# Kernel tuning notes

Measured on AMD Instinct MI355X. Metric: run time of the kernel, lower is better.

Reference implementation:

```python
import jax, jax.numpy as jnp
import numpy as np

S = 520   # WAP_SIZE / sequence length
E = 6     # EMBEDDING_SIZE
H = 3     # num_heads
D = 2     # head_dim
EPS = 1e-5


def _layer_norm(x, g, b):
    m = jnp.mean(x, axis=-1, keepdims=True)
    v = jnp.mean((x - m) ** 2, axis=-1, keepdims=True)
    return (x - m) * jax.lax.rsqrt(v + EPS) * g + b


def setup_inputs() -> dict:
    key = jax.random.key(0)
    ks = jax.random.split(key, 8)
    B = 256
    return {
        "x": jax.random.normal(ks[0], (B, S), dtype=jnp.float32),
        "Wq": jax.random.normal(ks[1], (E, E), dtype=jnp.float32),
        "Wk": jax.random.normal(ks[2], (E, E), dtype=jnp.float32),
        "Wv": jax.random.normal(ks[3], (E, E), dtype=jnp.float32),
        "Wo": jax.random.normal(ks[4], (E, E), dtype=jnp.float32),
        "ln1_g": jnp.ones((E,), jnp.float32),
        "ln1_b": jnp.zeros((E,), jnp.float32),
        "fc1_w": jax.random.normal(ks[5], (E, S * E), dtype=jnp.float32) * 0.02,
        "fc1_b": jnp.zeros((E,), jnp.float32),
        "ln2_g": jnp.ones((E,), jnp.float32),
        "ln2_b": jnp.zeros((E,), jnp.float32),
        "fc2_w": jax.random.normal(ks[6], (4, E), dtype=jnp.float32) * 0.1,
        "fc2_b": jnp.zeros((4,), jnp.float32),
    }


def reference(x, Wq, Wk, Wv, Wo, ln1_g, ln1_b, fc1_w, fc1_b, ln2_g, ln2_b, fc2_w, fc2_b):
    B = x.shape[0]
    # x: [B, S] -> broadcast to [B, S, E] (original: unsqueeze + expand)
    xe = jnp.broadcast_to(x[..., None], (B, S, E))
    Q = xe @ Wq  # [B, S, E]
    K = xe @ Wk
    V = xe @ Wv
    # split heads: [B, S, E] -> [B, H, S, D]
    def split(t):
        return t.reshape(B, S, H, D).transpose(0, 2, 1, 3)
    Qh, Kh, Vh = split(Q), split(K), split(V)
    scores = jnp.einsum('bhsd,bhtd->bhst', Qh, Kh) / jnp.sqrt(jnp.float32(D))
    attn = jax.nn.softmax(scores, axis=-1)            # [B, H, S, S]
    ctx = jnp.einsum('bhst,bhtd->bhsd', attn, Vh)     # [B, H, S, D]
    ctx = ctx.transpose(0, 2, 1, 3).reshape(B, S, H * D)  # [B, S, E]
    out = ctx @ Wo                                     # [B, S, E]
    out = _layer_norm(out, ln1_g, ln1_b)
    out = out.reshape(B, S * E)                        # [B, 3120]
    out = jax.nn.relu(out @ fc1_w.T + fc1_b)           # [B, E]
    out = _layer_norm(out, ln2_g, ln2_b)
    out = out @ fc2_w.T + fc2_b                        # [B, 4]
    return jax.nn.softmax(out, axis=-1)
```

## Files before the change

kernel.cpp:

```cpp
#include <hip/hip_runtime.h>
#include <math.h>

#define S_LEN 520
#define E_DIM 6
#define H_N   3
#define NPAIR (H_N * S_LEN)
#define K1_TPB 256
#define K1_BLKS 7
#define K2_TPB 256

typedef float f32x2 __attribute__((ext_vector_type(2)));

__device__ __forceinline__ float fast_exp2(float v) {
#if __has_builtin(__builtin_amdgcn_exp2f)
    return __builtin_amdgcn_exp2f(v);
#else
    return exp2f(v);
#endif
}

__device__ __forceinline__ f32x2 pk_fma(f32x2 a, f32x2 b, f32x2 c) {
    f32x2 d;
    asm("v_pk_fma_f32 %0, %1, %2, %3" : "=v"(d) : "v"(a), "v"(b), "v"(c));
    return d;
}
__device__ __forceinline__ f32x2 pk_add(f32x2 a, f32x2 b) {
    f32x2 d;
    asm("v_pk_add_f32 %0, %1, %2" : "=v"(d) : "v"(a), "v"(b));
    return d;
}

__global__ __launch_bounds__(K1_TPB, 1) void k1_pairs(
    const float* __restrict__ x,
    const float* __restrict__ Wq, const float* __restrict__ Wk,
    float* __restrict__ wls)
{
    const int b   = blockIdx.y;
    const int tid = threadIdx.x;

    __shared__ __align__(16) float xs[S_LEN];
    __shared__ float csh[H_N];
    __shared__ float qk[2][E_DIM];
    __shared__ float wredmx[K1_TPB / 64], wredmn[K1_TPB / 64];
    __shared__ float xmax_s, xmin_s;

    for (int i = tid; i < S_LEN; i += K1_TPB) xs[i] = x[b * S_LEN + i];

    if (tid < 2 * E_DIM) {
        const float* W = (tid < E_DIM) ? Wq : Wk;
        int e = (tid < E_DIM) ? tid : tid - E_DIM;
        float sum = 0.f;
        #pragma unroll
        for (int i = 0; i < E_DIM; ++i) sum += W[i * E_DIM + e];
        qk[tid / E_DIM][e] = sum;
    }
    __syncthreads();
    if (tid < H_N) {
        csh[tid] = (qk[0][2*tid] * qk[1][2*tid] + qk[0][2*tid+1] * qk[1][2*tid+1])
                   * 0.7071067811865476f;
    }

    float mx = -1e30f, mn = 1e30f;
    for (int i = tid; i < S_LEN; i += K1_TPB) {
        float v = xs[i];
        mx = fmaxf(mx, v);
        mn = fminf(mn, v);
    }
    for (int off = 32; off > 0; off >>= 1) {
        mx = fmaxf(mx, __shfl_down(mx, off));
        mn = fminf(mn, __shfl_down(mn, off));
    }
    if ((tid & 63) == 0) { wredmx[tid >> 6] = mx; wredmn[tid >> 6] = mn; }
    __syncthreads();
    if (tid == 0) {
        float a = wredmx[0], c = wredmn[0];
        for (int w = 1; w < K1_TPB / 64; ++w) {
            a = fmaxf(a, wredmx[w]);
            c = fminf(c, wredmn[w]);
        }
        xmax_s = a; xmin_s = c;
    }
    __syncthreads();

    const int p = blockIdx.x * K1_TPB + tid;
    if (p >= NPAIR) return;
    const int h = p / S_LEN;
    const int s = p - h * S_LEN;

    const float LOG2E = 1.4426950408889634f;
    float a  = csh[h] * xs[s];
    float a2 = a * LOG2E;
    float m2 = (a >= 0.f ? a * xmax_s : a * xmin_s) * LOG2E;

    const f32x2 a2p  = {a2, a2};
    const f32x2 nm2p = {-m2, -m2};

    const float4* xs4 = (const float4*)xs;

    f32x2 den0 = {0.f, 0.f}, den1 = {0.f, 0.f}, den2 = {0.f, 0.f}, den3 = {0.f, 0.f};
    f32x2 num0 = {0.f, 0.f}, num1 = {0.f, 0.f}, num2 = {0.f, 0.f}, num3 = {0.f, 0.f};

    for (int it = 0; it < S_LEN / 8; ++it) {
        float4 xa = xs4[2 * it];
        float4 xb = xs4[2 * it + 1];
        f32x2 x0 = {xa.x, xa.y};
        f32x2 x1 = {xa.z, xa.w};
        f32x2 x2 = {xb.x, xb.y};
        f32x2 x3 = {xb.z, xb.w};

        f32x2 g0 = pk_fma(a2p, x0, nm2p);
        f32x2 g1 = pk_fma(a2p, x1, nm2p);
        f32x2 g2 = pk_fma(a2p, x2, nm2p);
        f32x2 g3 = pk_fma(a2p, x3, nm2p);

        f32x2 e0 = { fast_exp2(g0.x), fast_exp2(g0.y) };
        f32x2 e1 = { fast_exp2(g1.x), fast_exp2(g1.y) };
        f32x2 e2 = { fast_exp2(g2.x), fast_exp2(g2.y) };
        f32x2 e3 = { fast_exp2(g3.x), fast_exp2(g3.y) };

        den0 = pk_add(den0, e0);
        den1 = pk_add(den1, e1);
        den2 = pk_add(den2, e2);
        den3 = pk_add(den3, e3);

        num0 = pk_fma(e0, x0, num0);
        num1 = pk_fma(e1, x1, num1);
        num2 = pk_fma(e2, x2, num2);
        num3 = pk_fma(e3, x3, num3);
    }

    f32x2 denp = pk_add(pk_add(den0, den1), pk_add(den2, den3));
    f32x2 nump = pk_add(pk_add(num0, num1), pk_add(num2, num3));
    float den = denp.x + denp.y;
    float num = nump.x + nump.y;
    wls[(b * H_N + h) * S_LEN + s] = num / den;
}

__global__ __launch_bounds__(K2_TPB, 1) void k2_tail(
    const float* __restrict__ wls,
    const float* __restrict__ Wv, const float* __restrict__ Wo,
    const float* __restrict__ ln1_g, const float* __restrict__ ln1_b,
    const float* __restrict__ fc1_w, const float* __restrict__ fc1_b,
    const float* __restrict__ ln2_g, const float* __restrict__ ln2_b,
    const float* __restrict__ fc2_w, const float* __restrict__ fc2_b,
    float* __restrict__ out)
{
    const int b   = blockIdx.x;
    const int tid = threadIdx.x;

    __shared__ float Msh[H_N][E_DIM];
    __shared__ float wred[K2_TPB / 64][E_DIM];
    __shared__ float g1[E_DIM], b1[E_DIM];

    if (tid == 0) {
        float vv[E_DIM];
        #pragma unroll
        for (int e = 0; e < E_DIM; ++e) {
            float v = 0.f;
            #pragma unroll
            for (int i = 0; i < E_DIM; ++i) v += Wv[i * E_DIM + e];
            vv[e] = v;
        }
        for (int h = 0; h < H_N; ++h)
            #pragma unroll
            for (int e = 0; e < E_DIM; ++e)
                Msh[h][e] = vv[2*h] * Wo[(2*h) * E_DIM + e]
                          + vv[2*h+1] * Wo[(2*h+1) * E_DIM + e];
    }
    if (tid < E_DIM) { g1[tid] = ln1_g[tid]; b1[tid] = ln1_b[tid]; }
    __syncthreads();

    float yacc[E_DIM] = {0.f, 0.f, 0.f, 0.f, 0.f, 0.f};
    const float* wb = wls + b * NPAIR;
    for (int s = tid; s < S_LEN; s += K2_TPB) {
        float w0 = wb[s], w1 = wb[S_LEN + s], w2 = wb[2 * S_LEN + s];
        float o[E_DIM];
        float mean = 0.f;
        #pragma unroll
        for (int e = 0; e < E_DIM; ++e) {
            o[e] = w0 * Msh[0][e] + w1 * Msh[1][e] + w2 * Msh[2][e];
            mean += o[e];
        }
        mean *= (1.f / E_DIM);
        float var = 0.f;
        #pragma unroll
        for (int e = 0; e < E_DIM; ++e) { float d = o[e] - mean; var += d * d; }
        var *= (1.f / E_DIM);
        float r = rsqrtf(var + 1e-5f);
        float ln[E_DIM];
        #pragma unroll
        for (int e = 0; e < E_DIM; ++e)
            ln[e] = (o[e] - mean) * r * g1[e] + b1[e];

        const float* wrow = fc1_w + s * E_DIM;
        #pragma unroll
        for (int i = 0; i < E_DIM; ++i) {
            const float* wr = wrow + i * (S_LEN * E_DIM);
            float acc = yacc[i];
            #pragma unroll
            for (int e = 0; e < E_DIM; ++e) acc = fmaf(ln[e], wr[e], acc);
            yacc[i] = acc;
        }
    }

    #pragma unroll
    for (int i = 0; i < E_DIM; ++i)
        for (int off = 32; off > 0; off >>= 1)
            yacc[i] += __shfl_down(yacc[i], off);
    if ((tid & 63) == 0) {
        #pragma unroll
        for (int i = 0; i < E_DIM; ++i) wred[tid >> 6][i] = yacc[i];
    }
    __syncthreads();

    if (tid == 0) {
        const float LOG2E = 1.4426950408889634f;
        float y[E_DIM];
        float mean = 0.f;
        #pragma unroll
        for (int i = 0; i < E_DIM; ++i) {
            float t = wred[0][i];
            for (int w = 1; w < K2_TPB / 64; ++w) t += wred[w][i];
            y[i] = fmaxf(t + fc1_b[i], 0.f);
            mean += y[i];
        }
        mean *= (1.f / E_DIM);
        float var = 0.f;
        #pragma unroll
        for (int i = 0; i < E_DIM; ++i) { float d = y[i] - mean; var += d * d; }
        var *= (1.f / E_DIM);
        float r = rsqrtf(var + 1e-5f);
        float l2[E_DIM];
        #pragma unroll
        for (int i = 0; i < E_DIM; ++i)
            l2[i] = (y[i] - mean) * r * ln2_g[i] + ln2_b[i];

        float z[4];
        float zmax = -1e30f;
        #pragma unroll
        for (int k = 0; k < 4; ++k) {
            float acc = fc2_b[k];
            #pragma unroll
            for (int i = 0; i < E_DIM; ++i)
                acc = fmaf(l2[i], fc2_w[k * E_DIM + i], acc);
            z[k] = acc;
            zmax = fmaxf(zmax, acc);
        }
        float ez[4];
        float se = 0.f;
        #pragma unroll
        for (int k = 0; k < 4; ++k) {
            ez[k] = fast_exp2((z[k] - zmax) * LOG2E);
            se += ez[k];
        }
        float inv = 1.f / se;
        #pragma unroll
        for (int k = 0; k < 4; ++k) out[b * 4 + k] = ez[k] * inv;
    }
}

#define TPB   320
#define NWAVE (TPB / 64)

__global__ __launch_bounds__(TPB, 1) void fused_tx_kernel(
    const float* __restrict__ x,
    const float* __restrict__ Wq, const float* __restrict__ Wk,
    const float* __restrict__ Wv, const float* __restrict__ Wo,
    const float* __restrict__ ln1_g, const float* __restrict__ ln1_b,
    const float* __restrict__ fc1_w, const float* __restrict__ fc1_b,
    const float* __restrict__ ln2_g, const float* __restrict__ ln2_b,
    const float* __restrict__ fc2_w, const float* __restrict__ fc2_b,
    float* __restrict__ out)
{
    const int b   = blockIdx.x;
    const int tid = threadIdx.x;

    __shared__ __align__(16) float xs[S_LEN];
    __shared__ float csh[H_N];
    __shared__ float Msh[H_N][E_DIM];
    __shared__ float wls[H_N][S_LEN];
    __shared__ float wred[NWAVE][2];
    __shared__ float xmax_s, xmin_s;
    __shared__ float ysum[E_DIM];

    for (int i = tid; i < S_LEN; i += TPB) xs[i] = x[b * S_LEN + i];
    if (tid < E_DIM) ysum[tid] = 0.f;

    if (tid == 0) {
        float qv[E_DIM], kv[E_DIM], vv[E_DIM];
        for (int e = 0; e < E_DIM; ++e) {
            float q = 0.f, k = 0.f, v = 0.f;
            for (int i = 0; i < E_DIM; ++i) {
                q += Wq[i * E_DIM + e];
                k += Wk[i * E_DIM + e];
                v += Wv[i * E_DIM + e];
            }
            qv[e] = q; kv[e] = k; vv[e] = v;
        }
        const float inv_sqrt_d = 0.7071067811865476f;
        for (int h = 0; h < H_N; ++h) {
            csh[h] = (qv[2*h] * kv[2*h] + qv[2*h+1] * kv[2*h+1]) * inv_sqrt_d;
            for (int e = 0; e < E_DIM; ++e)
                Msh[h][e] = vv[2*h] * Wo[(2*h) * E_DIM + e]
                          + vv[2*h+1] * Wo[(2*h+1) * E_DIM + e];
        }
    }
    __syncthreads();

    {
        float mx = -1e30f, mn = 1e30f;
        for (int i = tid; i < S_LEN; i += TPB) {
            float v = xs[i];
            mx = fmaxf(mx, v);
            mn = fminf(mn, v);
        }
        for (int off = 32; off > 0; off >>= 1) {
            mx = fmaxf(mx, __shfl_down(mx, off));
            mn = fminf(mn, __shfl_down(mn, off));
        }
        int wave = tid >> 6, lane = tid & 63;
        if (lane == 0) { wred[wave][0] = mx; wred[wave][1] = mn; }
        __syncthreads();
        if (tid == 0) {
            float a = wred[0][0], c = wred[0][1];
            for (int w = 1; w < NWAVE; ++w) {
                a = fmaxf(a, wred[w][0]);
                c = fminf(c, wred[w][1]);
            }
            xmax_s = a; xmin_s = c;
        }
        __syncthreads();
    }

    const float LOG2E = 1.4426950408889634f;
    const float xmax = xmax_s, xmin = xmin_s;
    const float4* xs4 = (const float4*)xs;

    for (int p = tid; p < NPAIR; p += TPB) {
        int h = p / S_LEN;
        int s = p - h * S_LEN;
        float a  = csh[h] * xs[s];
        float a2 = a * LOG2E;
        float m2 = (a >= 0.f ? a * xmax : a * xmin) * LOG2E;

        float den0 = 0.f, den1 = 0.f, den2 = 0.f, den3 = 0.f;
        float num0 = 0.f, num1 = 0.f, num2 = 0.f, num3 = 0.f;
        #pragma unroll 2
        for (int t4 = 0; t4 < S_LEN / 4; ++t4) {
            float4 xv = xs4[t4];
            float e0 = fast_exp2(fmaf(a2, xv.x, -m2));
            float e1 = fast_exp2(fmaf(a2, xv.y, -m2));
            float e2 = fast_exp2(fmaf(a2, xv.z, -m2));
            float e3 = fast_exp2(fmaf(a2, xv.w, -m2));
            den0 += e0; den1 += e1; den2 += e2; den3 += e3;
            num0 = fmaf(e0, xv.x, num0);
            num1 = fmaf(e1, xv.y, num1);
            num2 = fmaf(e2, xv.z, num2);
            num3 = fmaf(e3, xv.w, num3);
        }
        float den = (den0 + den1) + (den2 + den3);
        float num = (num0 + num1) + (num2 + num3);
        wls[h][s] = num / den;
    }
    __syncthreads();

    float yacc[E_DIM] = {0.f, 0.f, 0.f, 0.f, 0.f, 0.f};
    for (int s = tid; s < S_LEN; s += TPB) {
        float w0 = wls[0][s], w1 = wls[1][s], w2 = wls[2][s];
        float o[E_DIM];
        float mean = 0.f;
        #pragma unroll
        for (int e = 0; e < E_DIM; ++e) {
            o[e] = w0 * Msh[0][e] + w1 * Msh[1][e] + w2 * Msh[2][e];
            mean += o[e];
        }
        mean *= (1.f / E_DIM);
        float var = 0.f;
        #pragma unroll
        for (int e = 0; e < E_DIM; ++e) { float d = o[e] - mean; var += d * d; }
        var *= (1.f / E_DIM);
        float r = rsqrtf(var + 1e-5f);
        float ln[E_DIM];
        #pragma unroll
        for (int e = 0; e < E_DIM; ++e)
            ln[e] = (o[e] - mean) * r * ln1_g[e] + ln1_b[e];

        const float* wrow = fc1_w + s * E_DIM;
        #pragma unroll
        for (int i = 0; i < E_DIM; ++i) {
            const float* wr = wrow + i * (S_LEN * E_DIM);
            float acc = yacc[i];
            #pragma unroll
            for (int e = 0; e < E_DIM; ++e) acc = fmaf(ln[e], wr[e], acc);
            yacc[i] = acc;
        }
    }

    #pragma unroll
    for (int i = 0; i < E_DIM; ++i)
        for (int off = 32; off > 0; off >>= 1)
            yacc[i] += __shfl_down(yacc[i], off);
    if ((tid & 63) == 0) {
        #pragma unroll
        for (int i = 0; i < E_DIM; ++i) atomicAdd(&ysum[i], yacc[i]);
    }
    __syncthreads();

    if (tid == 0) {
        float y[E_DIM];
        float mean = 0.f;
        #pragma unroll
        for (int i = 0; i < E_DIM; ++i) {
            y[i] = fmaxf(ysum[i] + fc1_b[i], 0.f);
            mean += y[i];
        }
        mean *= (1.f / E_DIM);
        float var = 0.f;
        #pragma unroll
        for (int i = 0; i < E_DIM; ++i) { float d = y[i] - mean; var += d * d; }
        var *= (1.f / E_DIM);
        float r = rsqrtf(var + 1e-5f);
        float l2[E_DIM];
        #pragma unroll
        for (int i = 0; i < E_DIM; ++i)
            l2[i] = (y[i] - mean) * r * ln2_g[i] + ln2_b[i];

        float z[4];
        float zmax = -1e30f;
        #pragma unroll
        for (int k = 0; k < 4; ++k) {
            float acc = fc2_b[k];
            #pragma unroll
            for (int i = 0; i < E_DIM; ++i)
                acc = fmaf(l2[i], fc2_w[k * E_DIM + i], acc);
            z[k] = acc;
            zmax = fmaxf(zmax, acc);
        }
        float ez[4];
        float se = 0.f;
        #pragma unroll
        for (int k = 0; k < 4; ++k) {
            ez[k] = fast_exp2((z[k] - zmax) * LOG2E);
            se += ez[k];
        }
        float inv = 1.f / se;
        #pragma unroll
        for (int k = 0; k < 4; ++k) out[b * 4 + k] = ez[k] * inv;
    }
}

extern "C" void kernel_launch(void* const* d_in, const int* in_sizes, int n_in,
                              void* d_out, int out_size, void* d_ws, size_t ws_size,
                              hipStream_t stream) {
    const float* x     = (const float*)d_in[0];
    const float* Wq    = (const float*)d_in[1];
    const float* Wk    = (const float*)d_in[2];
    const float* Wv    = (const float*)d_in[3];
    const float* Wo    = (const float*)d_in[4];
    const float* ln1_g = (const float*)d_in[5];
    const float* ln1_b = (const float*)d_in[6];
    const float* fc1_w = (const float*)d_in[7];
    const float* fc1_b = (const float*)d_in[8];
    const float* ln2_g = (const float*)d_in[9];
    const float* ln2_b = (const float*)d_in[10];
    const float* fc2_w = (const float*)d_in[11];
    const float* fc2_b = (const float*)d_in[12];
    float* out = (float*)d_out;

    const int B = in_sizes[0] / S_LEN;
    const size_t need = (size_t)B * NPAIR * sizeof(float);

    if (ws_size >= need) {
        float* wls = (float*)d_ws;
        dim3 grid1(K1_BLKS, B);
        k1_pairs<<<grid1, K1_TPB, 0, stream>>>(x, Wq, Wk, wls);
        k2_tail<<<B, K2_TPB, 0, stream>>>(wls, Wv, Wo, ln1_g, ln1_b,
                                          fc1_w, fc1_b, ln2_g, ln2_b,
                                          fc2_w, fc2_b, out);
    } else {
        fused_tx_kernel<<<B, TPB, 0, stream>>>(
            x, Wq, Wk, Wv, Wo, ln1_g, ln1_b, fc1_w, fc1_b,
            ln2_g, ln2_b, fc2_w, fc2_b, out);
    }
}
```

Before: 38.42 us.

## Hoist per-row max/min and head constants into a separate stats kernel

Adds a small pre-kernel that computes each row's max and min of x and the per-head score constants (with log2e folded in) once, and writes them to workspace. The pair kernel then loads these instead of redoing the block-wide reduction, dropping two barriers and the redundant per-block weight sums. The pair kernel also moves to 512 threads and 4 blocks per row, uses a float4 load for x, and picks the head index by comparison instead of division. The cost is an extra kernel launch and a dependency between launches, and the 4×512 layout leaves more idle threads than 7×256 did (2048 vs 1792 slots for 1560 pairs).

```diff
diff --git a/kernel.cpp b/kernel.cpp
--- a/kernel.cpp
+++ b/kernel.cpp
@@ -5,8 +5,8 @@
 #define E_DIM 6
 #define H_N   3
 #define NPAIR (H_N * S_LEN)
-#define K1_TPB 256
-#define K1_BLKS 7
+#define K1_TPB 512
+#define K1_BLKS 4
 #define K2_TPB 256
 
 typedef float f32x2 __attribute__((ext_vector_type(2)));
@@ -30,67 +30,74 @@
     return d;
 }
 
-__global__ __launch_bounds__(K1_TPB, 1) void k1_pairs(
+
+__global__ __launch_bounds__(64, 1) void k0_stats(
     const float* __restrict__ x,
     const float* __restrict__ Wq, const float* __restrict__ Wk,
+    float2* __restrict__ stats, float* __restrict__ csh_out)
+{
+    const int b    = blockIdx.x;
+    const int lane = threadIdx.x;
+
+    float mx = -1e30f, mn = 1e30f;
+    const float* xr = x + b * S_LEN;
+    for (int i = lane; i < S_LEN; i += 64) {
+        float v = xr[i];
+        mx = fmaxf(mx, v);
+        mn = fminf(mn, v);
+    }
+    for (int off = 32; off > 0; off >>= 1) {
+        mx = fmaxf(mx, __shfl_down(mx, off));
+        mn = fminf(mn, __shfl_down(mn, off));
+    }
+    if (lane == 0) stats[b] = make_float2(mx, mn);
+
+    if (b == 0) {
+        __shared__ float qk[2][E_DIM];
+        if (lane < 2 * E_DIM) {
+            const float* W = (lane < E_DIM) ? Wq : Wk;
+            int e = (lane < E_DIM) ? lane : lane - E_DIM;
+            float sum = 0.f;
+            #pragma unroll
+            for (int i = 0; i < E_DIM; ++i) sum += W[i * E_DIM + e];
+            qk[lane / E_DIM][e] = sum;
+        }
+        __syncthreads();
+        if (lane < H_N) {
+            const float LOG2E = 1.4426950408889634f;
+            csh_out[lane] = (qk[0][2*lane] * qk[1][2*lane]
+                           + qk[0][2*lane+1] * qk[1][2*lane+1])
+                          * 0.7071067811865476f * LOG2E;
+        }
+    }
+}
+
+__global__ __launch_bounds__(K1_TPB, 8) void k1_pairs(
+    const float* __restrict__ x,
+    const float2* __restrict__ stats,
+    const float* __restrict__ csh,
     float* __restrict__ wls)
 {
     const int b   = blockIdx.y;
     const int tid = threadIdx.x;
 
     __shared__ __align__(16) float xs[S_LEN];
-    __shared__ float csh[H_N];
-    __shared__ float qk[2][E_DIM];
-    __shared__ float wredmx[K1_TPB / 64], wredmn[K1_TPB / 64];
-    __shared__ float xmax_s, xmin_s;
-
-    for (int i = tid; i < S_LEN; i += K1_TPB) xs[i] = x[b * S_LEN + i];
-
-    if (tid < 2 * E_DIM) {
-        const float* W = (tid < E_DIM) ? Wq : Wk;
-        int e = (tid < E_DIM) ? tid : tid - E_DIM;
-        float sum = 0.f;
-        #pragma unroll
-        for (int i = 0; i < E_DIM; ++i) sum += W[i * E_DIM + e];
-        qk[tid / E_DIM][e] = sum;
-    }
-    __syncthreads();
-    if (tid < H_N) {
-        csh[tid] = (qk[0][2*tid] * qk[1][2*tid] + qk[0][2*tid+1] * qk[1][2*tid+1])
-                   * 0.7071067811865476f;
-    }
-
-    float mx = -1e30f, mn = 1e30f;
-    for (int i = tid; i < S_LEN; i += K1_TPB) {
-        float v = xs[i];
-        mx = fmaxf(mx, v);
-        mn = fminf(mn, v);
-    }
-    for (int off = 32; off > 0; off >>= 1) {
-        mx = fmaxf(mx, __shfl_down(mx, off));
-        mn = fminf(mn, __shfl_down(mn, off));
-    }
-    if ((tid & 63) == 0) { wredmx[tid >> 6] = mx; wredmn[tid >> 6] = mn; }
-    __syncthreads();
-    if (tid == 0) {
-        float a = wredmx[0], c = wredmn[0];
-        for (int w = 1; w < K1_TPB / 64; ++w) {
-            a = fmaxf(a, wredmx[w]);
-            c = fminf(c, wredmn[w]);
-        }
-        xmax_s = a; xmin_s = c;
-    }
-    __syncthreads();
+
+    if (tid < S_LEN / 4)
+        ((float4*)xs)[tid] = ((const float4*)(x + b * S_LEN))[tid];
+
+    const float2 st = stats[b];
 
     const int p = blockIdx.x * K1_TPB + tid;
+    const int h = (p >= 2 * S_LEN) ? 2 : (p >= S_LEN ? 1 : 0);
+    const int s = p - h * S_LEN;
+    const float c = csh[h];
+
+    __syncthreads();
     if (p >= NPAIR) return;
-    const int h = p / S_LEN;
-    const int s = p - h * S_LEN;
-
-    const float LOG2E = 1.4426950408889634f;
-    float a  = csh[h] * xs[s];
-    float a2 = a * LOG2E;
-    float m2 = (a >= 0.f ? a * xmax_s : a * xmin_s) * LOG2E;
+
+    const float a2 = c * xs[s];
+    const float m2 = (a2 >= 0.f) ? a2 * st.x : a2 * st.y;
 
     const f32x2 a2p  = {a2, a2};
     const f32x2 nm2p = {-m2, -m2};
@@ -468,12 +475,18 @@
     float* out = (float*)d_out;
 
     const int B = in_sizes[0] / S_LEN;
-    const size_t need = (size_t)B * NPAIR * sizeof(float);
+    const size_t wls_bytes   = (size_t)B * NPAIR * sizeof(float);
+    const size_t stats_bytes = (size_t)B * sizeof(float2);
+    const size_t need = wls_bytes + stats_bytes + 4 * sizeof(float);
 
     if (ws_size >= need) {
-        float* wls = (float*)d_ws;
+        float*  wls   = (float*)d_ws;
+        float2* stats = (float2*)((char*)d_ws + wls_bytes);
+        float*  csh   = (float*)((char*)d_ws + wls_bytes + stats_bytes);
+
+        k0_stats<<<B, 64, 0, stream>>>(x, Wq, Wk, stats, csh);
         dim3 grid1(K1_BLKS, B);
-        k1_pairs<<<grid1, K1_TPB, 0, stream>>>(x, Wq, Wk, wls);
+        k1_pairs<<<grid1, K1_TPB, 0, stream>>>(x, stats, csh, wls);
         k2_tail<<<B, K2_TPB, 0, stream>>>(wls, Wv, Wo, ln1_g, ln1_b,
                                           fc1_w, fc1_b, ln2_g, ln2_b,
                                           fc2_w, fc2_b, out);
```

After: 46.51 us. 21.1% more time.

## Remove shared memory and block barriers from pair kernel, read x directly

Applied to the files above, without the earlier changes.

The pair kernel no longer stages the x row in LDS or uses block-wide barriers. Each wavefront computes the row max/min itself with xor shuffles, and every thread recomputes the per-head Q·K scale constants from the weights. The inner loop now reads x straight from global memory with uniform addresses, which should become scalar or broadcast cached loads. The launch bound drops the min-blocks hint. The aim is to cut barrier and LDS staging latency, at the cost of redundant global loads and reductions in every wave.

```diff
diff --git a/kernel.cpp b/kernel.cpp
--- a/kernel.cpp
+++ b/kernel.cpp
@@ -30,83 +30,67 @@
     return d;
 }
 
-__global__ __launch_bounds__(K1_TPB, 1) void k1_pairs(
+__global__ __launch_bounds__(K1_TPB) void k1_pairs(
     const float* __restrict__ x,
     const float* __restrict__ Wq, const float* __restrict__ Wk,
     float* __restrict__ wls)
 {
     const int b   = blockIdx.y;
     const int tid = threadIdx.x;
-
-    __shared__ __align__(16) float xs[S_LEN];
-    __shared__ float csh[H_N];
-    __shared__ float qk[2][E_DIM];
-    __shared__ float wredmx[K1_TPB / 64], wredmn[K1_TPB / 64];
-    __shared__ float xmax_s, xmin_s;
-
-    for (int i = tid; i < S_LEN; i += K1_TPB) xs[i] = x[b * S_LEN + i];
-
-    if (tid < 2 * E_DIM) {
-        const float* W = (tid < E_DIM) ? Wq : Wk;
-        int e = (tid < E_DIM) ? tid : tid - E_DIM;
-        float sum = 0.f;
-        #pragma unroll
-        for (int i = 0; i < E_DIM; ++i) sum += W[i * E_DIM + e];
-        qk[tid / E_DIM][e] = sum;
-    }
-    __syncthreads();
-    if (tid < H_N) {
-        csh[tid] = (qk[0][2*tid] * qk[1][2*tid] + qk[0][2*tid+1] * qk[1][2*tid+1])
-                   * 0.7071067811865476f;
-    }
+    const float* __restrict__ xrow = x + b * S_LEN;
 
     float mx = -1e30f, mn = 1e30f;
-    for (int i = tid; i < S_LEN; i += K1_TPB) {
-        float v = xs[i];
+    for (int i = (tid & 63); i < S_LEN; i += 64) {
+        float v = xrow[i];
         mx = fmaxf(mx, v);
         mn = fminf(mn, v);
     }
+    #pragma unroll
     for (int off = 32; off > 0; off >>= 1) {
-        mx = fmaxf(mx, __shfl_down(mx, off));
-        mn = fminf(mn, __shfl_down(mn, off));
-    }
-    if ((tid & 63) == 0) { wredmx[tid >> 6] = mx; wredmn[tid >> 6] = mn; }
-    __syncthreads();
-    if (tid == 0) {
-        float a = wredmx[0], c = wredmn[0];
-        for (int w = 1; w < K1_TPB / 64; ++w) {
-            a = fmaxf(a, wredmx[w]);
-            c = fminf(c, wredmn[w]);
-        }
-        xmax_s = a; xmin_s = c;
-    }
-    __syncthreads();
+        mx = fmaxf(mx, __shfl_xor(mx, off));
+        mn = fminf(mn, __shfl_xor(mn, off));
+    }
+
+    float c0, c1, c2;
+    {
+        const float SC = 0.7071067811865476f * 1.4426950408889634f;
+        float cs[H_N];
+        #pragma unroll
+        for (int h = 0; h < H_N; ++h) {
+            float q0 = 0.f, q1 = 0.f, k0 = 0.f, k1 = 0.f;
+            #pragma unroll
+            for (int i = 0; i < E_DIM; ++i) {
+                q0 += Wq[i * E_DIM + 2*h];
+                q1 += Wq[i * E_DIM + 2*h + 1];
+                k0 += Wk[i * E_DIM + 2*h];
+                k1 += Wk[i * E_DIM + 2*h + 1];
+            }
+            cs[h] = (q0 * k0 + q1 * k1) * SC;
+        }
+        c0 = cs[0]; c1 = cs[1]; c2 = cs[2];
+    }
 
     const int p = blockIdx.x * K1_TPB + tid;
     if (p >= NPAIR) return;
-    const int h = p / S_LEN;
+    const int h = (p >= 2 * S_LEN) ? 2 : (p >= S_LEN ? 1 : 0);
     const int s = p - h * S_LEN;
-
-    const float LOG2E = 1.4426950408889634f;
-    float a  = csh[h] * xs[s];
-    float a2 = a * LOG2E;
-    float m2 = (a >= 0.f ? a * xmax_s : a * xmin_s) * LOG2E;
+    const float c = (h == 0) ? c0 : (h == 1 ? c1 : c2);
+
+    const float a2 = c * xrow[s];
+    const float m2 = (a2 >= 0.f) ? a2 * mx : a2 * mn;
 
     const f32x2 a2p  = {a2, a2};
     const f32x2 nm2p = {-m2, -m2};
 
-    const float4* xs4 = (const float4*)xs;
-
     f32x2 den0 = {0.f, 0.f}, den1 = {0.f, 0.f}, den2 = {0.f, 0.f}, den3 = {0.f, 0.f};
     f32x2 num0 = {0.f, 0.f}, num1 = {0.f, 0.f}, num2 = {0.f, 0.f}, num3 = {0.f, 0.f};
 
     for (int it = 0; it < S_LEN / 8; ++it) {
-        float4 xa = xs4[2 * it];
-        float4 xb = xs4[2 * it + 1];
-        f32x2 x0 = {xa.x, xa.y};
-        f32x2 x1 = {xa.z, xa.w};
-        f32x2 x2 = {xb.x, xb.y};
-        f32x2 x3 = {xb.z, xb.w};
+        const float* __restrict__ xp = xrow + it * 8;
+        f32x2 x0 = {xp[0], xp[1]};
+        f32x2 x1 = {xp[2], xp[3]};
+        f32x2 x2 = {xp[4], xp[5]};
+        f32x2 x3 = {xp[6], xp[7]};
 
         f32x2 g0 = pk_fma(a2p, x0, nm2p);
         f32x2 g1 = pk_fma(a2p, x1, nm2p);
```

Result: slower. 43.27 us (+12.6%).
